# Kernel optimization log

Measured on AMD Instinct MI355X. Metric: run time of the kernel, lower is better.

Reference implementation:

```python
import jax, jax.numpy as jnp
import numpy as np


def _forward(x, conv_w, conv_b, lin_w, lin_b, W_in, conv1d_w, conv1d_b, W_x, W_dt, b_dt, A_log, Dp, W_out, We, be, Wa, ba, Wq, bq):
    B, _, H, Wd = x.shape
    E = conv_w.shape[0]
    # conv stem: Conv2d(k=3, pad=1) -> flatten(2) -> Linear(H*W -> img_size)
    z = jax.lax.conv_general_dilated(x, conv_w, (1, 1), [(1, 1), (1, 1)],
                                     dimension_numbers=('NCHW', 'OIHW', 'NCHW'))
    z = z + conv_b[None, :, None, None]
    z = z.reshape(B, E, H * Wd)                              # [B,E,HW]
    z = jnp.einsum('ben,mn->bem', z, lin_w) + lin_b          # [B,E,L]
    u = z.transpose(2, 0, 1)                                 # [L,B,E]: Mamba sees batch=L, seq=B
    # ---- Mamba block (mamba_ssm reference math) ----
    di = W_in.shape[0] // 2
    xz = u @ W_in.T                                          # [L,seq,2*di]
    xm, zg = xz[..., :di], xz[..., di:]
    K = conv1d_w.shape[-1]
    xc = jax.lax.conv_general_dilated(xm.transpose(0, 2, 1), conv1d_w, (1,), [(K - 1, 0)],
                                      dimension_numbers=('NCH', 'OIH', 'NCH'),
                                      feature_group_count=di)  # causal depthwise conv
    xs = jax.nn.silu((xc + conv1d_b[None, :, None]).transpose(0, 2, 1))  # [L,seq,di]
    dbl = xs @ W_x.T                                         # [L,seq,dt_rank+2S]
    dt_rank = W_dt.shape[1]
    S = A_log.shape[1]
    delta = jax.nn.softplus(dbl[..., :dt_rank] @ W_dt.T + b_dt)          # [L,seq,di]
    Bm = dbl[..., dt_rank:dt_rank + S]                       # [L,seq,S]
    Cm = dbl[..., dt_rank + S:]                              # [L,seq,S]
    A = -jnp.exp(A_log)                                      # [di,S]

    def step(h, t):
        d_t, b_t, c_t, x_t = t                               # [L,di],[L,S],[L,S],[L,di]
        h = jnp.exp(d_t[:, :, None] * A) * h + (d_t * x_t)[:, :, None] * b_t[:, None, :]
        return h, jnp.einsum('lds,ls->ld', h, c_t)

    h0 = jnp.zeros((u.shape[0], di, S), xs.dtype)
    _, ys = jax.lax.scan(step, h0, (delta.transpose(1, 0, 2), Bm.transpose(1, 0, 2),
                                    Cm.transpose(1, 0, 2), xs.transpose(1, 0, 2)))
    y = (ys.transpose(1, 0, 2) + xs * Dp) * jax.nn.silu(zg)  # [L,seq,di]
    out = y @ W_out.T                                        # [L,seq,E]
    feat = out[-1]                                           # [B,E] (last 'mamba batch' row)
    return feat @ We.T + be, feat @ Wa.T + ba, feat @ Wq.T + bq


def setup_inputs() -> dict:
    key = jax.random.key(0)
    ks = jax.random.split(key, 16)
    B, C, IMG, E, S, K = 512, 1, 32, 128, 256, 4
    di, dt_rank = 2 * E, 8
    sc = 0.02
    return {
        'x': jax.random.normal(ks[0], (B, C, IMG, IMG), jnp.float32),
        'conv_w': sc * jax.random.normal(ks[1], (E, C, 3, 3), jnp.float32),
        'conv_b': jnp.zeros((E,), jnp.float32),
        'lin_w': sc * jax.random.normal(ks[2], (IMG, IMG * IMG), jnp.float32),
        'lin_b': jnp.zeros((IMG,), jnp.float32),
        'W_in': sc * jax.random.normal(ks[3], (2 * di, E), jnp.float32),
        'conv1d_w': sc * jax.random.normal(ks[4], (di, 1, K), jnp.float32),
        'conv1d_b': jnp.zeros((di,), jnp.float32),
        'W_x': sc * jax.random.normal(ks[5], (dt_rank + 2 * S, di), jnp.float32),
        'W_dt': sc * jax.random.normal(ks[6], (di, dt_rank), jnp.float32),
        'b_dt': 0.1 * jax.random.normal(ks[7], (di,), jnp.float32),
        'A_log': jnp.log(jnp.broadcast_to(jnp.arange(1, S + 1, dtype=jnp.float32), (di, S))),
        'Dp': jnp.ones((di,), jnp.float32),
        'W_out': sc * jax.random.normal(ks[8], (E, di), jnp.float32),
        'We': sc * jax.random.normal(ks[9], (1, E), jnp.float32),
        'be': jnp.zeros((1,), jnp.float32),
        'Wa': sc * jax.random.normal(ks[10], (3, E), jnp.float32),
        'ba': jnp.zeros((3,), jnp.float32),
        'Wq': sc * jax.random.normal(ks[11], (4, E), jnp.float32),
        'bq': jnp.zeros((4,), jnp.float32),
    }


def reference(x, conv_w, conv_b, lin_w, lin_b, W_in, conv1d_w, conv1d_b, W_x, W_dt, b_dt, A_log, Dp, W_out, We, be, Wa, ba, Wq, bq):
    return _forward(x, conv_w, conv_b, lin_w, lin_b, W_in, conv1d_w, conv1d_b, W_x,
                    W_dt, b_dt, A_log, Dp, W_out, We, be, Wa, ba, Wq, bq)
```

## Files before the change

### kernel.cpp

```cpp
#include <hip/hip_runtime.h>
#include <math.h>

#define BATCH 512
#define E     128
#define DI    256
#define S     256
#define DTR   8
#define KCONV 4
#define JWX   520

__device__ __forceinline__ float silu_f(float v) {
    return v / (1.0f + __expf(-v));
}

__global__ __launch_bounds__(256) void kA_pre(
    const float* __restrict__ x, const float* __restrict__ conv_w,
    const float* __restrict__ conv_b, const float* __restrict__ lin_w,
    const float* __restrict__ lin_b, float* __restrict__ u31,
    const float* __restrict__ W_in, const float* __restrict__ W_x,
    const float* __restrict__ W_dt, const float* __restrict__ W_out,
    const float* __restrict__ c1w,
    float* __restrict__ W_inT, float* __restrict__ W_xT,
    float* __restrict__ W_dtT, float* __restrict__ W_outT,
    float* __restrict__ c1wT)
{
    const int tid = threadIdx.x;
    if (blockIdx.x >= 512) {
        const int bid = blockIdx.x - 512;
        const float* src; float* dst; int J, K, j0;
        if (bid < 9)       { src = W_x;   dst = W_xT;   J = JWX; K = DI;    j0 = bid * 64; }
        else if (bid < 17) { src = W_in;  dst = W_inT;  J = 512; K = E;     j0 = (bid - 9) * 64; }
        else if (bid < 19) { src = W_out; dst = W_outT; J = E;   K = DI;    j0 = (bid - 17) * 64; }
        else if (bid < 23) { src = W_dt;  dst = W_dtT;  J = DI;  K = DTR;   j0 = (bid - 19) * 64; }
        else               { src = c1w;   dst = c1wT;   J = DI;  K = KCONV; j0 = (bid - 23) * 64; }
        const int j = j0 + (tid & 63);
        if (j >= J) return;
        for (int c = tid >> 6; c < K; c += 4)
            dst[c * J + j] = src[j * K + c];
        return;
    }

    const int b = blockIdx.x;
    __shared__ float lw[1024];
    __shared__ float red[10][4];
    __shared__ float Tsh[10];

    const float4 lv = ((const float4*)(lin_w + 31 * 1024))[tid];
    ((float4*)lw)[tid] = lv;
    __syncthreads();

    float acc[10];
#pragma unroll
    for (int k = 0; k < 10; k++) acc[k] = 0.0f;

    const float4 xv = ((const float4*)(x + (size_t)b * 1024))[tid];
    const int p0 = tid * 4;
    const int h = p0 >> 5, w0 = p0 & 31;
    const float xa[4] = {xv.x, xv.y, xv.z, xv.w};
#pragma unroll
    for (int k = 0; k < 4; k++) {
        const float xval = xa[k];
        const int w = w0 + k;
#pragma unroll
        for (int i = 0; i < 3; i++) {
            const int hh = h - (i - 1);
            if (hh < 0 || hh > 31) continue;
#pragma unroll
            for (int j = 0; j < 3; j++) {
                const int ww = w - (j - 1);
                if (ww < 0 || ww > 31) continue;
                acc[i * 3 + j] += xval * lw[hh * 32 + ww];
            }
        }
    }
    acc[9] = lv.x + lv.y + lv.z + lv.w;

    const int wv = tid >> 6, ln = tid & 63;
#pragma unroll
    for (int k = 0; k < 10; k++) {
#pragma unroll
        for (int m = 1; m < 64; m <<= 1) acc[k] += __shfl_xor(acc[k], m, 64);
    }
    if (ln == 0) {
#pragma unroll
        for (int k = 0; k < 10; k++) red[k][wv] = acc[k];
    }
    __syncthreads();
    if (tid < 10) Tsh[tid] = red[tid][0] + red[tid][1] + red[tid][2] + red[tid][3];
    __syncthreads();

    if (tid < E) {
        const int e = tid;
        float v = lin_b[31] + conv_b[e] * Tsh[9];
#pragma unroll
        for (int k = 0; k < 9; k++) v += conv_w[e * 9 + k] * Tsh[k];
        u31[b * E + e] = v;
    }
}

__global__ __launch_bounds__(256) void k2a_win(
    const float* __restrict__ u31, const float* __restrict__ W_inT,
    float* __restrict__ xm, float* __restrict__ zg)
{
    const int bb = blockIdx.x * 4;
    const int tid = threadIdx.x;
    __shared__ float u[4][E];
    for (int i = tid; i < 4 * E; i += 256) u[i >> 7][i & 127] = u31[bb * E + i];
    __syncthreads();

    const int r = tid >> 6;
    const int j = blockIdx.y * 64 + (tid & 63);
    float a = 0.0f;
#pragma unroll 8
    for (int e = 0; e < E; e++) a += u[r][e] * W_inT[e * 512 + j];
    if (j < 256) xm[(bb + r) * DI + j] = a;
    else         zg[(bb + r) * DI + (j - 256)] = a;
}

__global__ __launch_bounds__(256) void k2b_conv_wx(
    const float* __restrict__ xm, const float* __restrict__ c1wT,
    const float* __restrict__ conv1d_b, const float* __restrict__ W_xT,
    const float* __restrict__ W_dtT, const float* __restrict__ b_dt,
    float* __restrict__ xs_g, float* __restrict__ delta_g,
    float* __restrict__ Bm, float* __restrict__ Cm)
{
    const int bb = blockIdx.x * 4;
    const int g = blockIdx.y;
    const int tid = threadIdx.x;
    __shared__ float xs[4][DI];
    __shared__ float dtin[4][8];

    for (int idx = tid; idx < 4 * DI; idx += 256) {
        const int r = idx >> 8, c = idx & 255;
        const int b = bb + r;
        float a = 0.0f;
#pragma unroll
        for (int k = 0; k < KCONV; k++) {
            const int src = b - 3 + k;
            if (src >= 0) a += xm[src * DI + c] * c1wT[k * DI + c];
        }
        a += conv1d_b[c];
        const float s = silu_f(a);
        xs[r][c] = s;
        if (g == 0) xs_g[b * DI + c] = s;
    }
    __syncthreads();

    const int r = tid >> 6;
    const int j = g * 64 + (tid & 63);
    if (j < JWX) {
        float a = 0.0f;
#pragma unroll 8
        for (int c = 0; c < DI; c++) a += xs[r][c] * W_xT[c * JWX + j];
        const int b = bb + r;
        if (j < DTR)          dtin[r][j] = a;
        else if (j < DTR + S) Bm[b * S + (j - DTR)] = a;
        else                  Cm[b * S + (j - DTR - S)] = a;
    }
    __syncthreads();

    if (g == 0) {
        const int d = tid;
        const float bd = b_dt[d];
#pragma unroll
        for (int r2 = 0; r2 < 4; r2++) {
            float a = bd;
#pragma unroll
            for (int q = 0; q < DTR; q++) a += dtin[r2][q] * W_dtT[q * DI + d];
            const float sp = (a > 20.0f) ? a : log1pf(__expf(a));
            delta_g[(bb + r2) * DI + d] = sp;
        }
    }
}

template <int NCv>
__global__ __launch_bounds__(256) void k3a_local(
    const float* __restrict__ A_log, const float* __restrict__ delta,
    const float* __restrict__ xs, const float* __restrict__ Bm,
    const float* __restrict__ Cm, float* __restrict__ y,
    float* __restrict__ hloc, float* __restrict__ Dchunk)
{
    constexpr int TCv = BATCH / NCv;
    const int tid = threadIdx.x;
    const int wv = tid >> 6, ln = tid & 63;
    const int d = blockIdx.x * 4 + wv;
    const int c = blockIdx.y;
    const int s0 = ln * 4;
    const int t0 = c * TCv;

    const float4 al = *(const float4*)(A_log + d * S + s0);
    float4 A;
    A.x = -__expf(al.x); A.y = -__expf(al.y);
    A.z = -__expf(al.z); A.w = -__expf(al.w);

    float4 h = make_float4(0.f, 0.f, 0.f, 0.f);
    float cd = 0.0f;
    float pr[8];

    for (int tb = 0; tb < TCv; tb += 8) {
#pragma unroll
        for (int i = 0; i < 8; i++) {
            const int tt = t0 + tb + i;
            const float dd = delta[tt * DI + d];
            cd += dd;
            const float u = dd * xs[tt * DI + d];
            const float4 B = *(const float4*)(Bm + tt * S + s0);
            const float4 C = *(const float4*)(Cm + tt * S + s0);
            h.x = __expf(dd * A.x) * h.x + u * B.x;
            h.y = __expf(dd * A.y) * h.y + u * B.y;
            h.z = __expf(dd * A.z) * h.z + u * B.z;
            h.w = __expf(dd * A.w) * h.w + u * B.w;
            pr[i] = h.x * C.x + h.y * C.y + h.z * C.z + h.w * C.w;
        }
#pragma unroll
        for (int i = 0; i < 8; i++) {
#pragma unroll
            for (int m = 1; m < 64; m <<= 1) pr[i] += __shfl_xor(pr[i], m, 64);
        }
        if (ln == 0) {
#pragma unroll
            for (int i = 0; i < 8; i++) y[(t0 + tb + i) * DI + d] = pr[i];
        }
    }

    *(float4*)(hloc + ((size_t)(c * DI + d)) * S + s0) = h;
    if (ln == 0) Dchunk[c * DI + d] = cd;
}

template <int NCv>
__global__ __launch_bounds__(256) void k3c_fix(
    const float* __restrict__ A_log, const float* __restrict__ delta,
    const float* __restrict__ Cm, const float* __restrict__ hloc,
    const float* __restrict__ Dchunk, float* __restrict__ y)
{
    constexpr int TCv = BATCH / NCv;
    const int tid = threadIdx.x;
    const int wv = tid >> 6, ln = tid & 63;
    const int d = blockIdx.x * 4 + wv;
    const int c = blockIdx.y + 1;
    const int s0 = ln * 4;
    const int t0 = c * TCv;

    const float4 al = *(const float4*)(A_log + d * S + s0);
    float4 A;
    A.x = -__expf(al.x); A.y = -__expf(al.y);
    A.z = -__expf(al.z); A.w = -__expf(al.w);

    float4 hi = make_float4(0.f, 0.f, 0.f, 0.f);
    for (int cp = 1; cp <= c; cp++) {
        const float4 hl = *(const float4*)(hloc + ((size_t)((cp - 1) * DI + d)) * S + s0);
        const float Dc = Dchunk[(cp - 1) * DI + d];
        hi.x = hl.x + __expf(A.x * Dc) * hi.x;
        hi.y = hl.y + __expf(A.y * Dc) * hi.y;
        hi.z = hl.z + __expf(A.z * Dc) * hi.z;
        hi.w = hl.w + __expf(A.w * Dc) * hi.w;
    }

    float cd = 0.0f;
    float pr[8];

    for (int tb = 0; tb < TCv; tb += 8) {
#pragma unroll
        for (int i = 0; i < 8; i++) {
            const int tt = t0 + tb + i;
            const float dd = delta[tt * DI + d];
            cd += dd;
            const float4 C = *(const float4*)(Cm + tt * S + s0);
            const float fx = hi.x * __expf(cd * A.x);
            const float fy = hi.y * __expf(cd * A.y);
            const float fz = hi.z * __expf(cd * A.z);
            const float fw = hi.w * __expf(cd * A.w);
            pr[i] = fx * C.x + fy * C.y + fz * C.z + fw * C.w;
        }
#pragma unroll
        for (int i = 0; i < 8; i++) {
#pragma unroll
            for (int m = 1; m < 64; m <<= 1) pr[i] += __shfl_xor(pr[i], m, 64);
        }
        if (ln == 0) {
#pragma unroll
            for (int i = 0; i < 8; i++) {
                const int tt = t0 + tb + i;
                y[tt * DI + d] += pr[i];
            }
        }
    }
}

__global__ __launch_bounds__(256) void k4_heads(
    const float* __restrict__ y, const float* __restrict__ xs,
    const float* __restrict__ Dp, const float* __restrict__ zg,
    const float* __restrict__ W_outT,
    const float* __restrict__ We, const float* __restrict__ be,
    const float* __restrict__ Wa, const float* __restrict__ ba,
    const float* __restrict__ Wq, const float* __restrict__ bq,
    float* __restrict__ out)
{
    const int bb = blockIdx.x * 2;
    const int tid = threadIdx.x;
    __shared__ float yf[2][DI];
    __shared__ float feat[2][E];

    for (int idx = tid; idx < 2 * DI; idx += 256) {
        const int r = idx >> 8, c = idx & 255;
        const int b = bb + r;
        const float z = zg[b * DI + c];
        yf[r][c] = (y[b * DI + c] + xs[b * DI + c] * Dp[c]) * silu_f(z);
    }
    __syncthreads();

    {
        const int r = tid >> 7, e = tid & 127;
        float a = 0.0f;
#pragma unroll 8
        for (int dd = 0; dd < DI; dd++) a += yf[r][dd] * W_outT[dd * E + e];
        feat[r][e] = a;
    }
    __syncthreads();

    if (tid < 16) {
        const int r = tid >> 3, hd = tid & 7;
        const int b = bb + r;
        const float* wrow;
        float bias;
        int dst;
        if (hd == 0)      { wrow = We;                 bias = be[0];      dst = b; }
        else if (hd < 4)  { wrow = Wa + (hd - 1) * E;  bias = ba[hd - 1]; dst = 512 + b * 3 + (hd - 1); }
        else              { wrow = Wq + (hd - 4) * E;  bias = bq[hd - 4]; dst = 2048 + b * 4 + (hd - 4); }
        float a = bias;
#pragma unroll 4
        for (int e = 0; e < E; e++) a += feat[r][e] * wrow[e];
        out[dst] = a;
    }
}

template <int NCv>
static void launch_scan(const float* A_log, const float* delta, const float* xs,
                        const float* Bm, const float* Cm, float* y,
                        float* hloc, float* Dchunk, hipStream_t stream)
{
    k3a_local<NCv><<<dim3(64, NCv), 256, 0, stream>>>(A_log, delta, xs, Bm, Cm, y, hloc, Dchunk);
    k3c_fix<NCv><<<dim3(64, NCv - 1), 256, 0, stream>>>(A_log, delta, Cm, hloc, Dchunk, y);
}

extern "C" void kernel_launch(void* const* d_in, const int* in_sizes, int n_in,
                              void* d_out, int out_size, void* d_ws, size_t ws_size,
                              hipStream_t stream)
{
    const float* x        = (const float*)d_in[0];
    const float* conv_w   = (const float*)d_in[1];
    const float* conv_b   = (const float*)d_in[2];
    const float* lin_w    = (const float*)d_in[3];
    const float* lin_b    = (const float*)d_in[4];
    const float* W_in     = (const float*)d_in[5];
    const float* conv1d_w = (const float*)d_in[6];
    const float* conv1d_b = (const float*)d_in[7];
    const float* W_x      = (const float*)d_in[8];
    const float* W_dt     = (const float*)d_in[9];
    const float* b_dt     = (const float*)d_in[10];
    const float* A_log    = (const float*)d_in[11];
    const float* Dp       = (const float*)d_in[12];
    const float* W_out    = (const float*)d_in[13];
    const float* We       = (const float*)d_in[14];
    const float* be       = (const float*)d_in[15];
    const float* Wa       = (const float*)d_in[16];
    const float* ba       = (const float*)d_in[17];
    const float* Wq       = (const float*)d_in[18];
    const float* bq       = (const float*)d_in[19];
    float* out = (float*)d_out;

    float* ws = (float*)d_ws;
    float* u31    = ws;
    float* xm     = u31    + 512 * 128;
    float* zg     = xm     + 512 * 256;
    float* xs     = zg     + 512 * 256;
    float* delta  = xs     + 512 * 256;
    float* Bm     = delta  + 512 * 256;
    float* Cm     = Bm     + 512 * 256;
    float* y      = Cm     + 512 * 256;
    float* W_inT  = y      + 512 * 256;
    float* W_xT   = W_inT  + 128 * 512;
    float* W_dtT  = W_xT   + 256 * JWX;
    float* W_outT = W_dtT  + 8 * 256;
    float* c1wT   = W_outT + 256 * 128;
    float* tail   = c1wT   + 4 * 256;

    const size_t base_floats = (size_t)(tail - ws);
    const size_t avail = ws_size / 4 - base_floats;

    kA_pre<<<539, 256, 0, stream>>>(x, conv_w, conv_b, lin_w, lin_b, u31,
                                    W_in, W_x, W_dt, W_out, conv1d_w,
                                    W_inT, W_xT, W_dtT, W_outT, c1wT);
    k2a_win<<<dim3(128, 8), 256, 0, stream>>>(u31, W_inT, xm, zg);
    k2b_conv_wx<<<dim3(128, 9), 256, 0, stream>>>(xm, c1wT, conv1d_b, W_xT, W_dtT, b_dt,
                                                  xs, delta, Bm, Cm);

    if (avail >= (size_t)32 * DI * S + 32 * DI) {
        float* hloc = tail;
        float* Dch  = hloc + (size_t)32 * DI * S;
        launch_scan<32>(A_log, delta, xs, Bm, Cm, y, hloc, Dch, stream);
    } else if (avail >= (size_t)16 * DI * S + 16 * DI) {
        float* hloc = tail;
        float* Dch  = hloc + (size_t)16 * DI * S;
        launch_scan<16>(A_log, delta, xs, Bm, Cm, y, hloc, Dch, stream);
    } else {
        float* hloc = tail;
        float* Dch  = hloc + (size_t)8 * DI * S;
        launch_scan<8>(A_log, delta, xs, Bm, Cm, y, hloc, Dch, stream);
    }

    k4_heads<<<256, 256, 0, stream>>>(y, xs, Dp, zg, W_outT, We, be, Wa, ba, Wq, bq, out);
}
```

Baseline: 183.0 us.

## Fuse W_in projection into stem kernel and restructure chunked scan into up/down passes

```diff
diff --git a/kernel.cpp b/kernel.cpp
--- a/kernel.cpp
+++ b/kernel.cpp
@@ -16,23 +16,17 @@
 __global__ __launch_bounds__(256) void kA_pre(
     const float* __restrict__ x, const float* __restrict__ conv_w,
     const float* __restrict__ conv_b, const float* __restrict__ lin_w,
-    const float* __restrict__ lin_b, float* __restrict__ u31,
-    const float* __restrict__ W_in, const float* __restrict__ W_x,
-    const float* __restrict__ W_dt, const float* __restrict__ W_out,
-    const float* __restrict__ c1w,
-    float* __restrict__ W_inT, float* __restrict__ W_xT,
-    float* __restrict__ W_dtT, float* __restrict__ W_outT,
-    float* __restrict__ c1wT)
+    const float* __restrict__ lin_b, const float* __restrict__ W_in,
+    const float* __restrict__ W_x, const float* __restrict__ W_out,
+    float* __restrict__ xm, float* __restrict__ zg,
+    float* __restrict__ W_xT, float* __restrict__ W_outT)
 {
     const int tid = threadIdx.x;
     if (blockIdx.x >= 512) {
         const int bid = blockIdx.x - 512;
         const float* src; float* dst; int J, K, j0;
-        if (bid < 9)       { src = W_x;   dst = W_xT;   J = JWX; K = DI;    j0 = bid * 64; }
-        else if (bid < 17) { src = W_in;  dst = W_inT;  J = 512; K = E;     j0 = (bid - 9) * 64; }
-        else if (bid < 19) { src = W_out; dst = W_outT; J = E;   K = DI;    j0 = (bid - 17) * 64; }
-        else if (bid < 23) { src = W_dt;  dst = W_dtT;  J = DI;  K = DTR;   j0 = (bid - 19) * 64; }
-        else               { src = c1w;   dst = c1wT;   J = DI;  K = KCONV; j0 = (bid - 23) * 64; }
+        if (bid < 9) { src = W_x;   dst = W_xT;   J = JWX; K = DI; j0 = bid * 64; }
+        else         { src = W_out; dst = W_outT; J = E;   K = DI; j0 = (bid - 9) * 64; }
         const int j = j0 + (tid & 63);
         if (j >= J) return;
         for (int c = tid >> 6; c < K; c += 4)
@@ -44,6 +38,7 @@
     __shared__ float lw[1024];
     __shared__ float red[10][4];
     __shared__ float Tsh[10];
+    __shared__ float u[E];
 
     const float4 lv = ((const float4*)(lin_w + 31 * 1024))[tid];
     ((float4*)lw)[tid] = lv;
@@ -94,33 +89,34 @@
         float v = lin_b[31] + conv_b[e] * Tsh[9];
 #pragma unroll
         for (int k = 0; k < 9; k++) v += conv_w[e * 9 + k] * Tsh[k];
-        u31[b * E + e] = v;
-    }
-}
-
-__global__ __launch_bounds__(256) void k2a_win(
-    const float* __restrict__ u31, const float* __restrict__ W_inT,
-    float* __restrict__ xm, float* __restrict__ zg)
-{
-    const int bb = blockIdx.x * 4;
-    const int tid = threadIdx.x;
-    __shared__ float u[4][E];
-    for (int i = tid; i < 4 * E; i += 256) u[i >> 7][i & 127] = u31[bb * E + i];
-    __syncthreads();
-
-    const int r = tid >> 6;
-    const int j = blockIdx.y * 64 + (tid & 63);
-    float a = 0.0f;
+        u[e] = v;
+    }
+    __syncthreads();
+
+    {
+        const float4* w0p = (const float4*)(W_in + (size_t)tid * E);
+        const float4* w1p = (const float4*)(W_in + (size_t)(tid + 256) * E);
+        float a0 = 0.0f;
 #pragma unroll 8
-    for (int e = 0; e < E; e++) a += u[r][e] * W_inT[e * 512 + j];
-    if (j < 256) xm[(bb + r) * DI + j] = a;
-    else         zg[(bb + r) * DI + (j - 256)] = a;
+        for (int e4 = 0; e4 < E / 4; e4++) {
+            const float4 w = w0p[e4];
+            a0 += u[4*e4]*w.x + u[4*e4+1]*w.y + u[4*e4+2]*w.z + u[4*e4+3]*w.w;
+        }
+        float a1 = 0.0f;
+#pragma unroll 8
+        for (int e4 = 0; e4 < E / 4; e4++) {
+            const float4 w = w1p[e4];
+            a1 += u[4*e4]*w.x + u[4*e4+1]*w.y + u[4*e4+2]*w.z + u[4*e4+3]*w.w;
+        }
+        xm[b * DI + tid] = a0;
+        zg[b * DI + tid] = a1;
+    }
 }
 
 __global__ __launch_bounds__(256) void k2b_conv_wx(
-    const float* __restrict__ xm, const float* __restrict__ c1wT,
+    const float* __restrict__ xm, const float* __restrict__ c1w,
     const float* __restrict__ conv1d_b, const float* __restrict__ W_xT,
-    const float* __restrict__ W_dtT, const float* __restrict__ b_dt,
+    const float* __restrict__ W_dt, const float* __restrict__ b_dt,
     float* __restrict__ xs_g, float* __restrict__ delta_g,
     float* __restrict__ Bm, float* __restrict__ Cm)
 {
@@ -133,13 +129,12 @@
     for (int idx = tid; idx < 4 * DI; idx += 256) {
         const int r = idx >> 8, c = idx & 255;
         const int b = bb + r;
-        float a = 0.0f;
-#pragma unroll
-        for (int k = 0; k < KCONV; k++) {
-            const int src = b - 3 + k;
-            if (src >= 0) a += xm[src * DI + c] * c1wT[k * DI + c];
-        }
-        a += conv1d_b[c];
+        const float4 wc = ((const float4*)c1w)[c];
+        float a = conv1d_b[c];
+        if (b >= 3) a += xm[(b - 3) * DI + c] * wc.x;
+        if (b >= 2) a += xm[(b - 2) * DI + c] * wc.y;
+        if (b >= 1) a += xm[(b - 1) * DI + c] * wc.z;
+        a += xm[b * DI + c] * wc.w;
         const float s = silu_f(a);
         xs[r][c] = s;
         if (g == 0) xs_g[b * DI + c] = s;
@@ -162,11 +157,13 @@
     if (g == 0) {
         const int d = tid;
         const float bd = b_dt[d];
+        const float4 wd0 = ((const float4*)(W_dt + d * DTR))[0];
+        const float4 wd1 = ((const float4*)(W_dt + d * DTR))[1];
 #pragma unroll
         for (int r2 = 0; r2 < 4; r2++) {
-            float a = bd;
-#pragma unroll
-            for (int q = 0; q < DTR; q++) a += dtin[r2][q] * W_dtT[q * DI + d];
+            float a = bd
+                + dtin[r2][0]*wd0.x + dtin[r2][1]*wd0.y + dtin[r2][2]*wd0.z + dtin[r2][3]*wd0.w
+                + dtin[r2][4]*wd1.x + dtin[r2][5]*wd1.y + dtin[r2][6]*wd1.z + dtin[r2][7]*wd1.w;
             const float sp = (a > 20.0f) ? a : log1pf(__expf(a));
             delta_g[(bb + r2) * DI + d] = sp;
         }
@@ -174,10 +171,9 @@
 }
 
 template <int NCv>
-__global__ __launch_bounds__(256) void k3a_local(
+__global__ __launch_bounds__(256) void k3u_up(
     const float* __restrict__ A_log, const float* __restrict__ delta,
     const float* __restrict__ xs, const float* __restrict__ Bm,
-    const float* __restrict__ Cm, float* __restrict__ y,
     float* __restrict__ hloc, float* __restrict__ Dchunk)
 {
     constexpr int TCv = BATCH / NCv;
@@ -195,7 +191,6 @@
 
     float4 h = make_float4(0.f, 0.f, 0.f, 0.f);
     float cd = 0.0f;
-    float pr[8];
 
     for (int tb = 0; tb < TCv; tb += 8) {
 #pragma unroll
@@ -203,6 +198,55 @@
             const int tt = t0 + tb + i;
             const float dd = delta[tt * DI + d];
             cd += dd;
+            const float u = dd * xs[tt * DI + d];
+            const float4 B = *(const float4*)(Bm + tt * S + s0);
+            h.x = __expf(dd * A.x) * h.x + u * B.x;
+            h.y = __expf(dd * A.y) * h.y + u * B.y;
+            h.z = __expf(dd * A.z) * h.z + u * B.z;
+            h.w = __expf(dd * A.w) * h.w + u * B.w;
+        }
+    }
+
+    *(float4*)(hloc + ((size_t)(c * DI + d)) * S + s0) = h;
+    if (ln == 0) Dchunk[c * DI + d] = cd;
+}
+
+template <int NCv>
+__global__ __launch_bounds__(256) void k3d_down(
+    const float* __restrict__ A_log, const float* __restrict__ delta,
+    const float* __restrict__ xs, const float* __restrict__ Bm,
+    const float* __restrict__ Cm, const float* __restrict__ hloc,
+    const float* __restrict__ Dchunk, float* __restrict__ y)
+{
+    constexpr int TCv = BATCH / NCv;
+    const int tid = threadIdx.x;
+    const int wv = tid >> 6, ln = tid & 63;
+    const int d = blockIdx.x * 4 + wv;
+    const int c = (NCv - 1) - blockIdx.y;
+    const int s0 = ln * 4;
+    const int t0 = c * TCv;
+
+    const float4 al = *(const float4*)(A_log + d * S + s0);
+    float4 A;
+    A.x = -__expf(al.x); A.y = -__expf(al.y);
+    A.z = -__expf(al.z); A.w = -__expf(al.w);
+
+    float4 h = make_float4(0.f, 0.f, 0.f, 0.f);
+    for (int cp = 1; cp <= c; cp++) {
+        const float4 hl = *(const float4*)(hloc + ((size_t)((cp - 1) * DI + d)) * S + s0);
+        const float Dc = Dchunk[(cp - 1) * DI + d];
+        h.x = hl.x + __expf(A.x * Dc) * h.x;
+        h.y = hl.y + __expf(A.y * Dc) * h.y;
+        h.z = hl.z + __expf(A.z * Dc) * h.z;
+        h.w = hl.w + __expf(A.w * Dc) * h.w;
+    }
+
+    float pr[8];
+    for (int tb = 0; tb < TCv; tb += 8) {
+#pragma unroll
+        for (int i = 0; i < 8; i++) {
+            const int tt = t0 + tb + i;
+            const float dd = delta[tt * DI + d];
             const float u = dd * xs[tt * DI + d];
             const float4 B = *(const float4*)(Bm + tt * S + s0);
             const float4 C = *(const float4*)(Cm + tt * S + s0);
@@ -220,69 +264,6 @@
         if (ln == 0) {
 #pragma unroll
             for (int i = 0; i < 8; i++) y[(t0 + tb + i) * DI + d] = pr[i];
-        }
-    }
-
-    *(float4*)(hloc + ((size_t)(c * DI + d)) * S + s0) = h;
-    if (ln == 0) Dchunk[c * DI + d] = cd;
-}
-
-template <int NCv>
-__global__ __launch_bounds__(256) void k3c_fix(
-    const float* __restrict__ A_log, const float* __restrict__ delta,
-    const float* __restrict__ Cm, const float* __restrict__ hloc,
-    const float* __restrict__ Dchunk, float* __restrict__ y)
-{
-    constexpr int TCv = BATCH / NCv;
-    const int tid = threadIdx.x;
-    const int wv = tid >> 6, ln = tid & 63;
-    const int d = blockIdx.x * 4 + wv;
-    const int c = blockIdx.y + 1;
-    const int s0 = ln * 4;
-    const int t0 = c * TCv;
-
-    const float4 al = *(const float4*)(A_log + d * S + s0);
-    float4 A;
-    A.x = -__expf(al.x); A.y = -__expf(al.y);
-    A.z = -__expf(al.z); A.w = -__expf(al.w);
-
-    float4 hi = make_float4(0.f, 0.f, 0.f, 0.f);
-    for (int cp = 1; cp <= c; cp++) {
-        const float4 hl = *(const float4*)(hloc + ((size_t)((cp - 1) * DI + d)) * S + s0);
-        const float Dc = Dchunk[(cp - 1) * DI + d];
-        hi.x = hl.x + __expf(A.x * Dc) * hi.x;
-        hi.y = hl.y + __expf(A.y * Dc) * hi.y;
-        hi.z = hl.z + __expf(A.z * Dc) * hi.z;
-        hi.w = hl.w + __expf(A.w * Dc) * hi.w;
-    }
-
-    float cd = 0.0f;
-    float pr[8];
-
-    for (int tb = 0; tb < TCv; tb += 8) {
-#pragma unroll
-        for (int i = 0; i < 8; i++) {
-            const int tt = t0 + tb + i;
-            const float dd = delta[tt * DI + d];
-            cd += dd;
-            const float4 C = *(const float4*)(Cm + tt * S + s0);
-            const float fx = hi.x * __expf(cd * A.x);
-            const float fy = hi.y * __expf(cd * A.y);
-            const float fz = hi.z * __expf(cd * A.z);
-            const float fw = hi.w * __expf(cd * A.w);
-            pr[i] = fx * C.x + fy * C.y + fz * C.z + fw * C.w;
-        }
-#pragma unroll
-        for (int i = 0; i < 8; i++) {
-#pragma unroll
-            for (int m = 1; m < 64; m <<= 1) pr[i] += __shfl_xor(pr[i], m, 64);
-        }
-        if (ln == 0) {
-#pragma unroll
-            for (int i = 0; i < 8; i++) {
-                const int tt = t0 + tb + i;
-                y[tt * DI + d] += pr[i];
-            }
         }
     }
 }
@@ -339,8 +320,8 @@
                         const float* Bm, const float* Cm, float* y,
                         float* hloc, float* Dchunk, hipStream_t stream)
 {
-    k3a_local<NCv><<<dim3(64, NCv), 256, 0, stream>>>(A_log, delta, xs, Bm, Cm, y, hloc, Dchunk);
-    k3c_fix<NCv><<<dim3(64, NCv - 1), 256, 0, stream>>>(A_log, delta, Cm, hloc, Dchunk, y);
+    k3u_up<NCv><<<dim3(64, NCv), 256, 0, stream>>>(A_log, delta, xs, Bm, hloc, Dchunk);
+    k3d_down<NCv><<<dim3(64, NCv), 256, 0, stream>>>(A_log, delta, xs, Bm, Cm, hloc, Dchunk, y);
 }
 
 extern "C" void kernel_launch(void* const* d_in, const int* in_sizes, int n_in,
@@ -370,29 +351,24 @@
     float* out = (float*)d_out;
 
     float* ws = (float*)d_ws;
-    float* u31    = ws;
-    float* xm     = u31    + 512 * 128;
+    float* xm     = ws;
     float* zg     = xm     + 512 * 256;
     float* xs     = zg     + 512 * 256;
     float* delta  = xs     + 512 * 256;
     float* Bm     = delta  + 512 * 256;
     float* Cm     = Bm     + 512 * 256;
     float* y      = Cm     + 512 * 256;
-    float* W_inT  = y      + 512 * 256;
-    float* W_xT   = W_inT  + 128 * 512;
-    float* W_dtT  = W_xT   + 256 * JWX;
-    float* W_outT = W_dtT  + 8 * 256;
-    float* c1wT   = W_outT + 256 * 128;
-    float* tail   = c1wT   + 4 * 256;
+    float* W_xT   = y      + 512 * 256;
+    float* W_outT = W_xT   + 256 * JWX;
+    float* tail   = W_outT + 256 * 128;
 
     const size_t base_floats = (size_t)(tail - ws);
     const size_t avail = ws_size / 4 - base_floats;
 
-    kA_pre<<<539, 256, 0, stream>>>(x, conv_w, conv_b, lin_w, lin_b, u31,
-                                    W_in, W_x, W_dt, W_out, conv1d_w,
-                                    W_inT, W_xT, W_dtT, W_outT, c1wT);
-    k2a_win<<<dim3(128, 8), 256, 0, stream>>>(u31, W_inT, xm, zg);
-    k2b_conv_wx<<<dim3(128, 9), 256, 0, stream>>>(xm, c1wT, conv1d_b, W_xT, W_dtT, b_dt,
+    kA_pre<<<523, 256, 0, stream>>>(x, conv_w, conv_b, lin_w, lin_b,
+                                    W_in, W_x, W_out,
+                                    xm, zg, W_xT, W_outT);
+    k2b_conv_wx<<<dim3(128, 9), 256, 0, stream>>>(xm, conv1d_w, conv1d_b, W_xT, W_dt, b_dt,
                                                   xs, delta, Bm, Cm);
 
     if (avail >= (size_t)32 * DI * S + 32 * DI) {
```

After: 184.5 us. No clear change (+0.8%).
